# Optimization experiments

Measured on AMD Instinct MI355X. Metric: run time of the kernel, lower is better.

Reference implementation:

```python
import jax, jax.numpy as jnp
import numpy as np

T, B, C, N, H = 4, 32, 384, 196, 12
D = C // H
HID = 1536
ALPHA = 4.0  # spikingjelly default sigmoid surrogate alpha
EPS = 1e-5   # BatchNorm eps
SCALE = 0.25

@jax.custom_vjp
def spike(x):
    return (x >= 0.0).astype(x.dtype)

def _spike_fwd(x):
    return (x >= 0.0).astype(x.dtype), x

def _spike_bwd(x, g):
    s = jax.nn.sigmoid(ALPHA * x)
    return (g * ALPHA * s * (1.0 - s),)

spike.defvjp(_spike_fwd, _spike_bwd)

def lif(x, thr=1.0, tau=2.0):
    # Multi-step LIF, hard reset to 0, detach_reset=True; x: (T, ...)
    def step(v, xt):
        v = v + (xt - v) / tau
        s = spike(v - thr)
        v = v * (1.0 - jax.lax.stop_gradient(s))
        return v, s
    _, out = jax.lax.scan(step, jnp.zeros_like(x[0]), x)
    return out

def conv_bn(x, w, b, g, beta, m, var):
    # 1x1 Conv1d (= channel matmul) + inference-form BatchNorm1d; x: (T,B,Cin,N), w: (Cout,Cin)
    y = jnp.einsum('tbcn,oc->tbon', x, w)
    if b is not None:
        y = y + b[:, None]
    inv = g * jax.lax.rsqrt(var + EPS)
    return y * inv[:, None] + (beta - m * inv)[:, None]

def _heads(t):
    # (T,B,C,N) -> (T,B,H,N,D), matching transpose(-1,-2).reshape(T,B,N,H,D).permute(0,1,3,2,4)
    return jnp.swapaxes(t, -1, -2).reshape(T, B, N, H, D).transpose(0, 1, 3, 2, 4)

def block_fwd(x, policy, wq, qg, qb, qm, qv, wk, kg, kb, km, kvv, wv, vg, vb, vm, vvv,
              wp, bp, pg, pb, pm, pv, w1, b1, g1, be1, m1, v1, w2, b2, g2, be2, m2, v2):
    q = _heads(lif(conv_bn(x, wq, None, qg, qb, qm, qv)))
    k = _heads(lif(conv_bn(x, wk, None, kg, kb, km, kvv)))
    v = _heads(lif(conv_bn(x, wv, None, vg, vb, vm, vvv)))
    attn = jnp.einsum('tbhnd,tbhmd->tbhnm', q, k)           # (T,B,H,N,N)
    pr = policy.reshape(T, B, 1, 1, N)
    eye = jnp.eye(N, dtype=x.dtype)
    attn = attn * (pr + (1.0 - pr) * eye)                   # attention_policy masking
    o = jnp.einsum('tbhnm,tbhmd->tbhnd', attn, v) * SCALE
    o = jnp.swapaxes(o, 3, 4).reshape(T, B, C, N)           # transpose(3,4).reshape(T,B,C,N)
    o = lif(o, thr=0.5)                                     # attn_lif v_threshold=0.5
    o = lif(conv_bn(o, wp, bp, pg, pb, pm, pv))             # proj conv+bn+lif
    x = x + o                                               # residual 1
    h = lif(conv_bn(x, w1, b1, g1, be1, m1, v1))            # MLP fc1
    h = lif(conv_bn(h, w2, b2, g2, be2, m2, v2))            # MLP fc2
    return x + h                                            # residual 2

def setup_inputs():
    key = jax.random.key(0)
    ks = iter(jax.random.split(key, 48))
    def nrm(shape, s=1.0):
        return jax.random.normal(next(ks), shape, jnp.float32) * s
    def uni(shape):
        return jax.random.uniform(next(ks), shape, jnp.float32, minval=0.5, maxval=1.5)
    inp = {}
    inp['x'] = nrm((T, B, C, N))
    inp['policy'] = (jax.random.uniform(next(ks), (T * B, N, 1)) > 0.3).astype(jnp.float32)
    inp.update({'wq': nrm((C, C), 0.05), 'qg': jnp.ones((C,)), 'qb': jnp.zeros((C,)), 'qm': nrm((C,), 0.1), 'qv': uni((C,))})
    inp.update({'wk': nrm((C, C), 0.05), 'kg': jnp.ones((C,)), 'kb': jnp.zeros((C,)), 'km': nrm((C,), 0.1), 'kvv': uni((C,))})
    inp.update({'wv': nrm((C, C), 0.05), 'vg': jnp.ones((C,)), 'vb': jnp.zeros((C,)), 'vm': nrm((C,), 0.1), 'vvv': uni((C,))})
    inp.update({'wp': nrm((C, C), 0.05), 'bp': jnp.zeros((C,)), 'pg': jnp.ones((C,)), 'pb': jnp.zeros((C,)), 'pm': nrm((C,), 0.1), 'pv': uni((C,))})
    inp.update({'w1': nrm((HID, C), 0.05), 'b1': jnp.zeros((HID,)), 'g1': jnp.ones((HID,)), 'be1': jnp.zeros((HID,)), 'm1': nrm((HID,), 0.1), 'v1': uni((HID,))})
    inp.update({'w2': nrm((C, HID), 0.05), 'b2': jnp.zeros((C,)), 'g2': jnp.ones((C,)), 'be2': jnp.zeros((C,)), 'm2': nrm((C,), 0.1), 'v2': uni((C,))})
    return inp

def reference(x, policy, wq, qg, qb, qm, qv, wk, kg, kb, km, kvv, wv, vg, vb, vm, vvv,
              wp, bp, pg, pb, pm, pv, w1, b1, g1, be1, m1, v1, w2, b2, g2, be2, m2, v2):
    return block_fwd(x, policy, wq, qg, qb, qm, qv, wk, kg, kb, km, kvv, wv, vg, vb, vm, vvv,
                     wp, bp, pg, pb, pm, pv, w1, b1, g1, be1, m1, v1, w2, b2, g2, be2, m2, v2)
```

## Files before the change

kernel.cpp:

```cpp
#include <hip/hip_runtime.h>
#include <cstdint>
#include <cstddef>

#define N_POS 196

typedef __attribute__((ext_vector_type(2))) float f32x2;

__device__ __forceinline__ void async_copy16(const float* g, float* l) {
    __builtin_amdgcn_global_load_lds(
        (const __attribute__((address_space(1))) uint32_t*)g,
        (__attribute__((address_space(3))) uint32_t*)l,
        16, 0, 0);
}

template<int CIN, bool USE_FMA, bool ACCUM>
__global__ __launch_bounds__(512, 4) void convbn_kernel(
    const float* __restrict__ X, const float* __restrict__ W,
    const float* __restrict__ Bi, const float* __restrict__ Ga,
    const float* __restrict__ Be, const float* __restrict__ Mu,
    const float* __restrict__ Va, float* __restrict__ Y, int Cout,
    int nb, int b0, int xlocal, int ylocal)
{
#pragma clang fp contract(off)
    constexpr int NCH = CIN / 16;
    __shared__ float lds[2 * 3136 + 2 * 1024];
    float* Xs = lds;
    float* Ws = lds + 6272;
    const int tid = threadIdx.x;
    const int l   = blockIdx.x;
    const int t   = l / nb;
    const int bl  = l - t * nb;
    const int tbg = t * 32 + b0 + bl;
    const int xtb = xlocal ? l : tbg;
    const int ytb = ylocal ? l : tbg;
    const int o0  = blockIdx.y * 64;
    const int n0  = tid & 63;
    const int obase = (tid >> 6) * 8;
    const int col3 = (n0 < 4) ? (n0 + 192) : 196;
    const float* Xtb = X + (size_t)xtb * CIN * N_POS;
    const float* Wp  = W + (size_t)o0 * CIN;

    f32x2 acc01[8], acc23[8];
    #pragma unroll
    for (int i = 0; i < 8; ++i) { acc01[i] = (f32x2)0.f; acc23[i] = (f32x2)0.f; }

    auto stage = [&](int buf, int kc) {
        const int oo = tid >> 3, k2 = (tid & 7) * 2;
        float2 wv2 = *(const float2*)(Wp + (size_t)oo * CIN + kc + k2);
        {
            int i = tid;
            async_copy16(Xtb + (size_t)(kc + i / 49) * N_POS + (i % 49) * 4,
                         &Xs[buf * 3136 + (i & ~63) * 4]);
        }
        if (tid < 272) {
            int i = tid + 512;
            async_copy16(Xtb + (size_t)(kc + i / 49) * N_POS + (i % 49) * 4,
                         &Xs[buf * 3136 + (i & ~63) * 4]);
        }
        Ws[buf * 1024 + k2 * 64 + oo]       = wv2.x;
        Ws[buf * 1024 + (k2 + 1) * 64 + oo] = wv2.y;
    };

    stage(0, 0);
    __syncthreads();
    int buf = 0;
    for (int ch = 0; ch < NCH; ++ch) {
        if (ch + 1 < NCH) stage(buf ^ 1, (ch + 1) * 16);
        const float* Xb = Xs + buf * 3136;
        const float* Wb = Ws + buf * 1024;
        #pragma unroll
        for (int kk = 0; kk < 16; ++kk) {
            float4 wA = *(const float4*)(Wb + kk * 64 + obase);
            float4 wB = *(const float4*)(Wb + kk * 64 + obase + 4);
            f32x2 x01 = { Xb[kk * 196 + n0],       Xb[kk * 196 + n0 + 64] };
            f32x2 x23 = { Xb[kk * 196 + n0 + 128], Xb[kk * 196 + col3] };
            float w8[8] = { wA.x, wA.y, wA.z, wA.w, wB.x, wB.y, wB.z, wB.w };
            #pragma unroll
            for (int i = 0; i < 8; ++i) {
                f32x2 wd = { w8[i], w8[i] };
                if (USE_FMA) {
                    acc01[i] = __builtin_elementwise_fma(wd, x01, acc01[i]);
                    acc23[i] = __builtin_elementwise_fma(wd, x23, acc23[i]);
                } else {
                    acc01[i] = acc01[i] + wd * x01;
                    acc23[i] = acc23[i] + wd * x23;
                }
            }
        }
        __syncthreads();
        buf ^= 1;
    }

    #pragma unroll
    for (int i = 0; i < 8; ++i) {
        int o = o0 + obase + i;
        float sc = __fmul_rn(Ga[o], 1.0f / sqrtf(__fadd_rn(Va[o], 1e-5f)));
        float sh = __fsub_rn(Be[o], __fmul_rn(Mu[o], sc));
        float* yp = Y + ((size_t)ytb * Cout + o) * N_POS;
        float a[4] = { acc01[i].x, acc01[i].y, acc23[i].x, acc23[i].y };
        #pragma unroll
        for (int j = 0; j < 4; ++j) {
            if (j == 3 && n0 >= 4) continue;
            float y = a[j];
            if (Bi) y = __fadd_rn(y, Bi[o]);
            float r = __fadd_rn(__fmul_rn(y, sc), sh);
            int n = n0 + j * 64;
            if (ACCUM) yp[n] = __fadd_rn(yp[n], r);
            else       yp[n] = r;
        }
    }
}

__global__ __launch_bounds__(256) void lif_kernel(float* __restrict__ Y, int plane4, float thr)
{
    int idx = blockIdx.x * 256 + threadIdx.x;
    if (idx >= plane4) return;
    float4* Yp = (float4*)Y;
    float v0 = 0.f, v1 = 0.f, v2 = 0.f, v3 = 0.f;
    #pragma unroll
    for (int t = 0; t < 4; ++t) {
        float4 xv = Yp[(size_t)t * plane4 + idx];
        v0 = __fadd_rn(v0, __fmul_rn(__fsub_rn(xv.x, v0), 0.5f));
        v1 = __fadd_rn(v1, __fmul_rn(__fsub_rn(xv.y, v1), 0.5f));
        v2 = __fadd_rn(v2, __fmul_rn(__fsub_rn(xv.z, v2), 0.5f));
        v3 = __fadd_rn(v3, __fmul_rn(__fsub_rn(xv.w, v3), 0.5f));
        float s0 = (__fsub_rn(v0, thr) >= 0.f) ? 1.f : 0.f;
        float s1 = (__fsub_rn(v1, thr) >= 0.f) ? 1.f : 0.f;
        float s2 = (__fsub_rn(v2, thr) >= 0.f) ? 1.f : 0.f;
        float s3 = (__fsub_rn(v3, thr) >= 0.f) ? 1.f : 0.f;
        v0 = __fmul_rn(v0, 1.f - s0); v1 = __fmul_rn(v1, 1.f - s1);
        v2 = __fmul_rn(v2, 1.f - s2); v3 = __fmul_rn(v3, 1.f - s3);
        xv.x = s0; xv.y = s1; xv.z = s2; xv.w = s3;
        Yp[(size_t)t * plane4 + idx] = xv;
    }
}

__global__ __launch_bounds__(256) void lif_add_kernel(
    const float* __restrict__ Yin, float* __restrict__ Out, int b0)
{
    const int PL4 = 8 * 384 * 49;
    const int B4  = 384 * 49;
    int idx = blockIdx.x * 256 + threadIdx.x;
    if (idx >= PL4) return;
    int bl = idx / B4, r = idx - bl * B4;
    const float4* Yp = (const float4*)Yin;
    float v0 = 0.f, v1 = 0.f, v2 = 0.f, v3 = 0.f;
    #pragma unroll
    for (int t = 0; t < 4; ++t) {
        float4 xv = Yp[(size_t)t * PL4 + idx];
        v0 = __fadd_rn(v0, __fmul_rn(__fsub_rn(xv.x, v0), 0.5f));
        v1 = __fadd_rn(v1, __fmul_rn(__fsub_rn(xv.y, v1), 0.5f));
        v2 = __fadd_rn(v2, __fmul_rn(__fsub_rn(xv.z, v2), 0.5f));
        v3 = __fadd_rn(v3, __fmul_rn(__fsub_rn(xv.w, v3), 0.5f));
        float s0 = (__fsub_rn(v0, 1.0f) >= 0.f) ? 1.f : 0.f;
        float s1 = (__fsub_rn(v1, 1.0f) >= 0.f) ? 1.f : 0.f;
        float s2 = (__fsub_rn(v2, 1.0f) >= 0.f) ? 1.f : 0.f;
        float s3 = (__fsub_rn(v3, 1.0f) >= 0.f) ? 1.f : 0.f;
        v0 = __fmul_rn(v0, 1.f - s0); v1 = __fmul_rn(v1, 1.f - s1);
        v2 = __fmul_rn(v2, 1.f - s2); v3 = __fmul_rn(v3, 1.f - s3);
        float4* op = (float4*)Out + ((size_t)(t * 32 + b0 + bl) * B4 + r);
        float4 o = *op;
        o.x = __fadd_rn(o.x, s0); o.y = __fadd_rn(o.y, s1);
        o.z = __fadd_rn(o.z, s2); o.w = __fadd_rn(o.w, s3);
        *op = o;
    }
}

__global__ __launch_bounds__(256) void pack_kernel(const float* __restrict__ S,
                                                   uint32_t* __restrict__ Bits)
{
    int idx = blockIdx.x * 256 + threadIdx.x;
    if (idx >= 4 * 32 * 12 * 196) return;
    int n = idx % 196;
    int rest = idx / 196;
    int h = rest % 12;
    int tb = rest / 12;
    const float* sp = S + ((size_t)tb * 384 + h * 32) * 196 + n;
    uint32_t bits = 0;
    #pragma unroll
    for (int d = 0; d < 32; ++d)
        bits |= (sp[(size_t)d * 196] > 0.5f) ? (1u << d) : 0u;
    Bits[idx] = bits;
}

__global__ __launch_bounds__(256) void attn_kernel(
    const uint32_t* __restrict__ Qb, const uint32_t* __restrict__ Kb,
    const float* __restrict__ V, const float* __restrict__ P, float* __restrict__ O)
{
    __shared__ uint32_t Qbs[196], Kbs[196];
    __shared__ float Ps[196];
    __shared__ float Vs[32][204];
    __shared__ float Ss[32][204];
    __shared__ float Os[32][36];
    const int tid = threadIdx.x;
    const int bid = blockIdx.x;
    const int tb = bid / 12, h = bid - tb * 12;
    const size_t vbase = ((size_t)tb * 384 + h * 32) * 196;
    const size_t qbase = ((size_t)tb * 12 + h) * 196;
    for (int i = tid; i < 196; i += 256) {
        Qbs[i] = Qb[qbase + i];
        Kbs[i] = Kb[qbase + i];
        Ps[i]  = P[(size_t)tb * 196 + i];
    }
    for (int i = tid; i < 32 * 49; i += 256) {
        int d = i / 49, m4 = i - d * 49;
        *(float4*)&Vs[d][m4 * 4] = *(const float4*)(V + vbase + (size_t)d * 196 + m4 * 4);
    }
    __syncthreads();
    for (int n0 = 0; n0 < 196; n0 += 32) {
        const int rows = min(32, 196 - n0);
        for (int idx = tid; idx < rows * 196; idx += 256) {
            int ns = idx / 196, m = idx - ns * 196;
            int n = n0 + ns;
            float s = (float)__popc(Qbs[n] & Kbs[m]);
            float p = Ps[m];
            float e = (m == n) ? 1.f : 0.f;
            Ss[ns][m] = s * (p + (1.f - p) * e);
        }
        __syncthreads();
        {
            const int tn = tid & 15, td = tid >> 4;
            float a00 = 0, a01 = 0, a10 = 0, a11 = 0;
            #pragma unroll 7
            for (int m4 = 0; m4 < 49; ++m4) {
                float4 s0 = *(const float4*)&Ss[tn][m4 * 4];
                float4 s1 = *(const float4*)&Ss[tn + 16][m4 * 4];
                float4 u0 = *(const float4*)&Vs[td][m4 * 4];
                float4 u1 = *(const float4*)&Vs[td + 16][m4 * 4];
                a00 += s0.x * u0.x + s0.y * u0.y + s0.z * u0.z + s0.w * u0.w;
                a01 += s0.x * u1.x + s0.y * u1.y + s0.z * u1.z + s0.w * u1.w;
                a10 += s1.x * u0.x + s1.y * u0.y + s1.z * u0.z + s1.w * u0.w;
                a11 += s1.x * u1.x + s1.y * u1.y + s1.z * u1.z + s1.w * u1.w;
            }
            Os[td     ][tn     ] = a00 * 0.25f;
            Os[td + 16][tn     ] = a01 * 0.25f;
            Os[td     ][tn + 16] = a10 * 0.25f;
            Os[td + 16][tn + 16] = a11 * 0.25f;
        }
        __syncthreads();
        {
            const int d = tid >> 3, c4 = tid & 7;
            if (c4 * 4 < rows)
                *(float4*)(O + vbase + (size_t)d * 196 + n0 + c4 * 4) =
                    *(const float4*)&Os[d][c4 * 4];
        }
        __syncthreads();
    }
}

__global__ __launch_bounds__(256) void add_kernel(const float* __restrict__ A,
    const float* __restrict__ B, float* __restrict__ Out, int n4)
{
    int idx = blockIdx.x * 256 + threadIdx.x;
    if (idx >= n4) return;
    float4 a = ((const float4*)A)[idx];
    float4 b = ((const float4*)B)[idx];
    float4 o;
    o.x = __fadd_rn(a.x, b.x); o.y = __fadd_rn(a.y, b.y);
    o.z = __fadd_rn(a.z, b.z); o.w = __fadd_rn(a.w, b.w);
    ((float4*)Out)[idx] = o;
}

extern "C" void kernel_launch(void* const* d_in, const int* in_sizes, int n_in,
                              void* d_out, int out_size, void* d_ws, size_t ws_size,
                              hipStream_t stream) {
    const float* x   = (const float*)d_in[0];
    const float* pol = (const float*)d_in[1];
    const float* wq = (const float*)d_in[2];
    const float* qg = (const float*)d_in[3];
    const float* qb = (const float*)d_in[4];
    const float* qm = (const float*)d_in[5];
    const float* qv = (const float*)d_in[6];
    const float* wk = (const float*)d_in[7];
    const float* kg = (const float*)d_in[8];
    const float* kb = (const float*)d_in[9];
    const float* km = (const float*)d_in[10];
    const float* kvv= (const float*)d_in[11];
    const float* wv = (const float*)d_in[12];
    const float* vg = (const float*)d_in[13];
    const float* vb = (const float*)d_in[14];
    const float* vm = (const float*)d_in[15];
    const float* vvv= (const float*)d_in[16];
    const float* wp = (const float*)d_in[17];
    const float* bp = (const float*)d_in[18];
    const float* pg = (const float*)d_in[19];
    const float* pb = (const float*)d_in[20];
    const float* pm = (const float*)d_in[21];
    const float* pv = (const float*)d_in[22];
    const float* w1 = (const float*)d_in[23];
    const float* b1 = (const float*)d_in[24];
    const float* g1 = (const float*)d_in[25];
    const float* be1= (const float*)d_in[26];
    const float* m1 = (const float*)d_in[27];
    const float* v1 = (const float*)d_in[28];
    const float* w2 = (const float*)d_in[29];
    const float* b2 = (const float*)d_in[30];
    const float* g2 = (const float*)d_in[31];
    const float* be2= (const float*)d_in[32];
    const float* m2 = (const float*)d_in[33];
    const float* v2 = (const float*)d_in[34];

    float* bufA = (float*)d_ws;
    float* bufD = bufA + 9633792;
    uint32_t* Qbits = (uint32_t*)(bufD + 2408448);
    uint32_t* Kbits = Qbits + 301056;
    float* out = (float*)d_out;

    convbn_kernel<384, false, false><<<dim3(128, 6), 512, 0, stream>>>(x, wq, nullptr, qg, qb, qm, qv, bufA, 384, 32, 0, 0, 0);
    lif_kernel<<<2352, 256, 0, stream>>>(bufA, 602112, 1.0f);
    pack_kernel<<<1176, 256, 0, stream>>>(bufA, Qbits);
    convbn_kernel<384, false, false><<<dim3(128, 6), 512, 0, stream>>>(x, wk, nullptr, kg, kb, km, kvv, bufA, 384, 32, 0, 0, 0);
    lif_kernel<<<2352, 256, 0, stream>>>(bufA, 602112, 1.0f);
    pack_kernel<<<1176, 256, 0, stream>>>(bufA, Kbits);
    convbn_kernel<384, false, false><<<dim3(128, 6), 512, 0, stream>>>(x, wv, nullptr, vg, vb, vm, vvv, bufA, 384, 32, 0, 0, 0);
    lif_kernel<<<2352, 256, 0, stream>>>(bufA, 602112, 1.0f);

    attn_kernel<<<1536, 256, 0, stream>>>(Qbits, Kbits, bufA, pol, out);
    lif_kernel<<<2352, 256, 0, stream>>>(out, 602112, 0.5f);

    convbn_kernel<384, true, false><<<dim3(128, 6), 512, 0, stream>>>(out, wp, bp, pg, pb, pm, pv, bufA, 384, 32, 0, 0, 0);
    lif_kernel<<<2352, 256, 0, stream>>>(bufA, 602112, 1.0f);
    add_kernel<<<9408, 256, 0, stream>>>(x, bufA, out, 2408448);

    for (int c = 0; c < 4; ++c) {
        convbn_kernel<384, false, false><<<dim3(32, 24), 512, 0, stream>>>(out, w1, b1, g1, be1, m1, v1, bufA, 1536, 8, c * 8, 0, 1);
        lif_kernel<<<2352, 256, 0, stream>>>(bufA, 602112, 1.0f);
        convbn_kernel<1536, true, false><<<dim3(32, 6), 512, 0, stream>>>(bufA, w2, b2, g2, be2, m2, v2, bufD, 384, 8, c * 8, 1, 1);
        lif_add_kernel<<<588, 256, 0, stream>>>(bufD, out, c * 8);
    }
}
```

Measured before the change: 2.654 ms.

## Retile conv-BN kernel to 256 threads with 8x8 register tiles and vector I/O

```diff
diff --git a/kernel.cpp b/kernel.cpp
--- a/kernel.cpp
+++ b/kernel.cpp
@@ -4,7 +4,7 @@
 
 #define N_POS 196
 
-typedef __attribute__((ext_vector_type(2))) float f32x2;
+typedef __attribute__((ext_vector_type(4))) float f32x4;
 
 __device__ __forceinline__ void async_copy16(const float* g, float* l) {
     __builtin_amdgcn_global_load_lds(
@@ -14,7 +14,7 @@
 }
 
 template<int CIN, bool USE_FMA, bool ACCUM>
-__global__ __launch_bounds__(512, 4) void convbn_kernel(
+__global__ __launch_bounds__(256, 4) void convbn_kernel(
     const float* __restrict__ X, const float* __restrict__ W,
     const float* __restrict__ Bi, const float* __restrict__ Ga,
     const float* __restrict__ Be, const float* __restrict__ Mu,
@@ -34,31 +34,29 @@
     const int xtb = xlocal ? l : tbg;
     const int ytb = ylocal ? l : tbg;
     const int o0  = blockIdx.y * 64;
-    const int n0  = tid & 63;
-    const int obase = (tid >> 6) * 8;
-    const int col3 = (n0 < 4) ? (n0 + 192) : 196;
+    const int o   = tid & 31;
+    const int grp = tid >> 5;
     const float* Xtb = X + (size_t)xtb * CIN * N_POS;
     const float* Wp  = W + (size_t)o0 * CIN;
 
-    f32x2 acc01[8], acc23[8];
-    #pragma unroll
-    for (int i = 0; i < 8; ++i) { acc01[i] = (f32x2)0.f; acc23[i] = (f32x2)0.f; }
+    f32x4 accA[8], accB[8];
+    #pragma unroll
+    for (int i = 0; i < 8; ++i) { accA[i] = (f32x4)0.f; accB[i] = (f32x4)0.f; }
 
     auto stage = [&](int buf, int kc) {
-        const int oo = tid >> 3, k2 = (tid & 7) * 2;
-        float2 wv2 = *(const float2*)(Wp + (size_t)oo * CIN + kc + k2);
-        {
-            int i = tid;
-            async_copy16(Xtb + (size_t)(kc + i / 49) * N_POS + (i % 49) * 4,
-                         &Xs[buf * 3136 + (i & ~63) * 4]);
-        }
-        if (tid < 272) {
-            int i = tid + 512;
-            async_copy16(Xtb + (size_t)(kc + i / 49) * N_POS + (i % 49) * 4,
-                         &Xs[buf * 3136 + (i & ~63) * 4]);
-        }
-        Ws[buf * 1024 + k2 * 64 + oo]       = wv2.x;
-        Ws[buf * 1024 + (k2 + 1) * 64 + oo] = wv2.y;
+        const int oo = tid >> 2, k4 = tid & 3;
+        float4 wv4 = *(const float4*)(Wp + (size_t)oo * CIN + kc + k4 * 4);
+        #pragma unroll
+        for (int j = 0; j < 4; ++j) {
+            int i = tid + j * 256;
+            if (i < 784)
+                async_copy16(Xtb + (size_t)(kc + i / 49) * N_POS + (i % 49) * 4,
+                             &Xs[buf * 3136 + (i & ~63) * 4]);
+        }
+        Ws[buf * 1024 + (k4 * 4 + 0) * 64 + oo] = wv4.x;
+        Ws[buf * 1024 + (k4 * 4 + 1) * 64 + oo] = wv4.y;
+        Ws[buf * 1024 + (k4 * 4 + 2) * 64 + oo] = wv4.z;
+        Ws[buf * 1024 + (k4 * 4 + 3) * 64 + oo] = wv4.w;
     };
 
     stage(0, 0);
@@ -66,24 +64,24 @@
     int buf = 0;
     for (int ch = 0; ch < NCH; ++ch) {
         if (ch + 1 < NCH) stage(buf ^ 1, (ch + 1) * 16);
-        const float* Xb = Xs + buf * 3136;
-        const float* Wb = Ws + buf * 1024;
+        const float* Xb = Xs + buf * 3136 + o * 4;
+        const float* Wb = Ws + buf * 1024 + grp * 8;
         #pragma unroll
         for (int kk = 0; kk < 16; ++kk) {
-            float4 wA = *(const float4*)(Wb + kk * 64 + obase);
-            float4 wB = *(const float4*)(Wb + kk * 64 + obase + 4);
-            f32x2 x01 = { Xb[kk * 196 + n0],       Xb[kk * 196 + n0 + 64] };
-            f32x2 x23 = { Xb[kk * 196 + n0 + 128], Xb[kk * 196 + col3] };
+            f32x4 xA = *(const f32x4*)(Xb + kk * 196);
+            f32x4 xB = *(const f32x4*)(Xb + kk * 196 + 128);
+            float4 wA = *(const float4*)(Wb + kk * 64);
+            float4 wB = *(const float4*)(Wb + kk * 64 + 4);
             float w8[8] = { wA.x, wA.y, wA.z, wA.w, wB.x, wB.y, wB.z, wB.w };
             #pragma unroll
             for (int i = 0; i < 8; ++i) {
-                f32x2 wd = { w8[i], w8[i] };
+                f32x4 wd = { w8[i], w8[i], w8[i], w8[i] };
                 if (USE_FMA) {
-                    acc01[i] = __builtin_elementwise_fma(wd, x01, acc01[i]);
-                    acc23[i] = __builtin_elementwise_fma(wd, x23, acc23[i]);
+                    accA[i] = __builtin_elementwise_fma(wd, xA, accA[i]);
+                    accB[i] = __builtin_elementwise_fma(wd, xB, accB[i]);
                 } else {
-                    acc01[i] = acc01[i] + wd * x01;
-                    acc23[i] = acc23[i] + wd * x23;
+                    accA[i] = accA[i] + wd * xA;
+                    accB[i] = accB[i] + wd * xB;
                 }
             }
         }
@@ -93,20 +91,44 @@
 
     #pragma unroll
     for (int i = 0; i < 8; ++i) {
-        int o = o0 + obase + i;
-        float sc = __fmul_rn(Ga[o], 1.0f / sqrtf(__fadd_rn(Va[o], 1e-5f)));
-        float sh = __fsub_rn(Be[o], __fmul_rn(Mu[o], sc));
-        float* yp = Y + ((size_t)ytb * Cout + o) * N_POS;
-        float a[4] = { acc01[i].x, acc01[i].y, acc23[i].x, acc23[i].y };
-        #pragma unroll
-        for (int j = 0; j < 4; ++j) {
-            if (j == 3 && n0 >= 4) continue;
-            float y = a[j];
-            if (Bi) y = __fadd_rn(y, Bi[o]);
-            float r = __fadd_rn(__fmul_rn(y, sc), sh);
-            int n = n0 + j * 64;
-            if (ACCUM) yp[n] = __fadd_rn(yp[n], r);
-            else       yp[n] = r;
+        int oo = o0 + grp * 8 + i;
+        float sc = __fmul_rn(Ga[oo], 1.0f / sqrtf(__fadd_rn(Va[oo], 1e-5f)));
+        float sh = __fsub_rn(Be[oo], __fmul_rn(Mu[oo], sc));
+        float bi = Bi ? Bi[oo] : 0.f;
+        float* yp = Y + ((size_t)ytb * Cout + oo) * N_POS;
+        {
+            float a[4] = { accA[i].x, accA[i].y, accA[i].z, accA[i].w };
+            float4 r;
+            float* rp = &r.x;
+            #pragma unroll
+            for (int j = 0; j < 4; ++j) {
+                float y = Bi ? __fadd_rn(a[j], bi) : a[j];
+                rp[j] = __fadd_rn(__fmul_rn(y, sc), sh);
+            }
+            float* dst = yp + o * 4;
+            if (ACCUM) {
+                float4 y0 = *(const float4*)dst;
+                r.x = __fadd_rn(y0.x, r.x); r.y = __fadd_rn(y0.y, r.y);
+                r.z = __fadd_rn(y0.z, r.z); r.w = __fadd_rn(y0.w, r.w);
+            }
+            *(float4*)dst = r;
+        }
+        if (o <= 16) {
+            float a[4] = { accB[i].x, accB[i].y, accB[i].z, accB[i].w };
+            float4 r;
+            float* rp = &r.x;
+            #pragma unroll
+            for (int j = 0; j < 4; ++j) {
+                float y = Bi ? __fadd_rn(a[j], bi) : a[j];
+                rp[j] = __fadd_rn(__fmul_rn(y, sc), sh);
+            }
+            float* dst = yp + 128 + o * 4;
+            if (ACCUM) {
+                float4 y0 = *(const float4*)dst;
+                r.x = __fadd_rn(y0.x, r.x); r.y = __fadd_rn(y0.y, r.y);
+                r.z = __fadd_rn(y0.z, r.z); r.w = __fadd_rn(y0.w, r.w);
+            }
+            *(float4*)dst = r;
         }
     }
 }
@@ -306,26 +328,26 @@
     uint32_t* Kbits = Qbits + 301056;
     float* out = (float*)d_out;
 
-    convbn_kernel<384, false, false><<<dim3(128, 6), 512, 0, stream>>>(x, wq, nullptr, qg, qb, qm, qv, bufA, 384, 32, 0, 0, 0);
+    convbn_kernel<384, false, false><<<dim3(128, 6), 256, 0, stream>>>(x, wq, nullptr, qg, qb, qm, qv, bufA, 384, 32, 0, 0, 0);
     lif_kernel<<<2352, 256, 0, stream>>>(bufA, 602112, 1.0f);
     pack_kernel<<<1176, 256, 0, stream>>>(bufA, Qbits);
-    convbn_kernel<384, false, false><<<dim3(128, 6), 512, 0, stream>>>(x, wk, nullptr, kg, kb, km, kvv, bufA, 384, 32, 0, 0, 0);
+    convbn_kernel<384, false, false><<<dim3(128, 6), 256, 0, stream>>>(x, wk, nullptr, kg, kb, km, kvv, bufA, 384, 32, 0, 0, 0);
     lif_kernel<<<2352, 256, 0, stream>>>(bufA, 602112, 1.0f);
     pack_kernel<<<1176, 256, 0, stream>>>(bufA, Kbits);
-    convbn_kernel<384, false, false><<<dim3(128, 6), 512, 0, stream>>>(x, wv, nullptr, vg, vb, vm, vvv, bufA, 384, 32, 0, 0, 0);
+    convbn_kernel<384, false, false><<<dim3(128, 6), 256, 0, stream>>>(x, wv, nullptr, vg, vb, vm, vvv, bufA, 384, 32, 0, 0, 0);
     lif_kernel<<<2352, 256, 0, stream>>>(bufA, 602112, 1.0f);
 
     attn_kernel<<<1536, 256, 0, stream>>>(Qbits, Kbits, bufA, pol, out);
     lif_kernel<<<2352, 256, 0, stream>>>(out, 602112, 0.5f);
 
-    convbn_kernel<384, true, false><<<dim3(128, 6), 512, 0, stream>>>(out, wp, bp, pg, pb, pm, pv, bufA, 384, 32, 0, 0, 0);
+    convbn_kernel<384, true, false><<<dim3(128, 6), 256, 0, stream>>>(out, wp, bp, pg, pb, pm, pv, bufA, 384, 32, 0, 0, 0);
     lif_kernel<<<2352, 256, 0, stream>>>(bufA, 602112, 1.0f);
     add_kernel<<<9408, 256, 0, stream>>>(x, bufA, out, 2408448);
 
     for (int c = 0; c < 4; ++c) {
-        convbn_kernel<384, false, false><<<dim3(32, 24), 512, 0, stream>>>(out, w1, b1, g1, be1, m1, v1, bufA, 1536, 8, c * 8, 0, 1);
+        convbn_kernel<384, false, false><<<dim3(32, 24), 256, 0, stream>>>(out, w1, b1, g1, be1, m1, v1, bufA, 1536, 8, c * 8, 0, 1);
         lif_kernel<<<2352, 256, 0, stream>>>(bufA, 602112, 1.0f);
-        convbn_kernel<1536, true, false><<<dim3(32, 6), 512, 0, stream>>>(bufA, w2, b2, g2, be2, m2, v2, bufD, 384, 8, c * 8, 1, 1);
+        convbn_kernel<1536, true, false><<<dim3(32, 6), 256, 0, stream>>>(bufA, w2, b2, g2, be2, m2, v2, bufD, 384, 8, c * 8, 1, 1);
         lif_add_kernel<<<588, 256, 0, stream>>>(bufD, out, c * 8);
     }
 }
```

Result: faster. 2.411 ms (-9.1%).
